# Performance work log

Hardware: AMD Instinct MI355X
Metric: run time of the kernel (lower is better)

The kernel has to match this reference:

```python
import jax, jax.numpy as jnp
import numpy as np

NUM_HEADS = 8
EMBED = 512
HEAD_DIM = EMBED // NUM_HEADS
B, S = 4, 2048


def setup_inputs() -> dict:
    key = jax.random.key(0)
    ks = jax.random.split(key, 8)
    sc = 0.02
    return {
        "values": jax.random.normal(ks[0], (B, S, EMBED), dtype=jnp.float32),
        "keys": jax.random.normal(ks[1], (B, S, EMBED), dtype=jnp.float32),
        "query": jax.random.normal(ks[2], (B, S, EMBED), dtype=jnp.float32),
        "Wv": jax.random.normal(ks[3], (HEAD_DIM, HEAD_DIM), dtype=jnp.float32) * sc,
        "Wk": jax.random.normal(ks[4], (HEAD_DIM, HEAD_DIM), dtype=jnp.float32) * sc,
        "Wq": jax.random.normal(ks[5], (HEAD_DIM, HEAD_DIM), dtype=jnp.float32) * sc,
        "Wo": jax.random.normal(ks[6], (EMBED, EMBED), dtype=jnp.float32) * sc,
        "bo": jnp.zeros((EMBED,), dtype=jnp.float32),
    }


def reference(values, keys, query, Wv, Wk, Wq, Wo, bo):
    b, s, _ = query.shape
    # split heads: [B, S, H, D]
    v = values.reshape(b, s, NUM_HEADS, HEAD_DIM)
    k = keys.reshape(b, s, NUM_HEADS, HEAD_DIM)
    q = query.reshape(b, s, NUM_HEADS, HEAD_DIM)
    # per-head linear (nn.Linear: x @ W.T), weights shared across heads
    v = jnp.einsum("bshd,ed->bshe", v, Wv)
    k = jnp.einsum("bshd,ed->bshe", k, Wk)
    q = jnp.einsum("bshd,ed->bshe", q, Wq)
    # energy: [B, H, Q, K]
    energy = jnp.einsum("bqhd,bkhd->bhqk", q, k)
    # NOTE: original scales by sqrt(embed_size), not sqrt(head_dim)
    attn = jax.nn.softmax(energy / jnp.sqrt(jnp.float32(EMBED)), axis=-1)
    out = jnp.einsum("bhqk,bkhd->bqhd", attn, v).reshape(b, s, EMBED)
    return out @ Wo.T + bo
```

## Files before the change

### kernel.cpp

```cpp
#include <hip/hip_runtime.h>

#define H 8
#define D 64
#define E 512
#define BATCH 4
#define SEQ 2048

typedef __bf16 bf16v8 __attribute__((ext_vector_type(8)));
typedef float f32v4 __attribute__((ext_vector_type(4)));
typedef unsigned int u32v4 __attribute__((ext_vector_type(4)));
typedef unsigned short u16v4 __attribute__((ext_vector_type(4)));

#define MFMA16(a,b,c) __builtin_amdgcn_mfma_f32_16x16x32_bf16(a,b,c,0,0,0)

#define AS1 __attribute__((address_space(1)))
#define AS3 __attribute__((address_space(3)))
#define GLDS16(g, l) __builtin_amdgcn_global_load_lds((const AS1 void*)(g), (AS3 void*)(l), 16, 0, 0)

static __device__ __forceinline__ unsigned short f2bf(float f) {
  unsigned u = __builtin_bit_cast(unsigned, f);
  u += 0x7fffu + ((u >> 16) & 1u);
  return (unsigned short)(u >> 16);
}

static __device__ __forceinline__ float exp2_hw(float x) {
#if __has_builtin(__builtin_amdgcn_exp2f)
  return __builtin_amdgcn_exp2f(x);
#else
  return exp2f(x);
#endif
}

static __device__ __forceinline__ bf16v8 lds16(const char* p) {
  return __builtin_bit_cast(bf16v8, *(const u32v4*)p);
}

__global__ void prep_w(const float* __restrict__ Wo, const float* __restrict__ Wv,
                       const float* __restrict__ Wq, const float* __restrict__ Wk,
                       unsigned short* __restrict__ Wo2, unsigned short* __restrict__ MT) {
  int bx = blockIdx.x;
  if (bx < 1024) {
    int i = bx * 256 + threadIdx.x;
    int n = i >> 9, c = i & 511;
    int h = c >> 6, d = c & 63;
    float acc = 0.f;
    for (int e = 0; e < 64; ++e) acc += Wo[n*512 + h*64 + e] * Wv[e*64 + d];
    Wo2[n*512 + c] = f2bf(acc);
  } else {
    int i = (bx - 1024) * 256 + threadIdx.x;
    int d2 = i >> 6, d1 = i & 63;
    float acc = 0.f;
    for (int e = 0; e < 64; ++e) acc += Wq[e*64 + d1] * Wk[e*64 + d2];
    MT[d2*64 + d1] = f2bf(acc * 0.04419417382415922f);
  }
}

__global__ void prep_tok(const float* __restrict__ v, const float* __restrict__ keys,
                         unsigned short* __restrict__ vT, unsigned short* __restrict__ kb) {
  __shared__ float tile[64][65];
  int bh = blockIdx.y;
  int b = bh >> 3, h = bh & 7;
  int sc = blockIdx.x;
  int t = threadIdx.x;
  int flat = bh * 32 + sc;
  {
    const float* kp = keys + (size_t)flat * 4096;
    unsigned short* ko = kb + (size_t)flat * 4096;
    #pragma unroll
    for (int i = 0; i < 4; ++i) {
      f32v4 x = *(const f32v4*)(kp + (i*256 + t)*4);
      u16v4 o = { f2bf(x[0]), f2bf(x[1]), f2bf(x[2]), f2bf(x[3]) };
      *(u16v4*)(ko + (i*256 + t)*4) = o;
    }
  }
  #pragma unroll
  for (int i = 0; i < 16; ++i) {
    int idx = i*256 + t; int si = idx >> 6, d = idx & 63;
    tile[si][d] = v[((size_t)(b*SEQ + sc*64 + si))*E + h*64 + d];
  }
  __syncthreads();
  #pragma unroll
  for (int i = 0; i < 16; ++i) {
    int idx = i*256 + t; int d = idx >> 6, si = idx & 63;
    vT[((size_t)(bh*64 + d))*SEQ + sc*64 + si] = f2bf(tile[si][d]);
  }
}

__global__ __launch_bounds__(256, 4) void attn(const float* __restrict__ query,
                                               const unsigned short* __restrict__ MT,
                                               const unsigned short* __restrict__ kb,
                                               const unsigned short* __restrict__ vT,
                                               unsigned short* __restrict__ ao) {
  __shared__ __align__(16) char lds[40960];
  int bh = blockIdx.y, b = bh >> 3, h = bh & 7;
  int qt = blockIdx.x;
  int tid = threadIdx.x, w = tid >> 6, lane = tid & 63, hi = lane >> 4, lo = lane & 15;
  char* pw = lds + 32768 + w*2048;

  const unsigned short* kbase = kb + (size_t)(b*SEQ)*E + h*64;
  const unsigned short* vbase = vT + (size_t)bh*64*SEQ;

  int srow = tid >> 3, scc = tid & 7;

  #pragma unroll
  for (int i = 0; i < 2; ++i) {
    int row = i*32 + srow;
    int sc = scc ^ (row & 7);
    GLDS16(kbase + (size_t)row*E + sc*8,   lds        + i*4096 + w*1024);
    GLDS16(vbase + (size_t)row*SEQ + sc*8, lds + 8192 + i*4096 + w*1024);
  }
  {
    char* xl = lds + 16384;
    char* ml = lds + 24576;
    #pragma unroll
    for (int i = 0; i < 4; ++i) {
      int c = i*256 + tid;
      int row = c >> 4, cc = c & 15;
      f32v4 xv = *(const f32v4*)(query + (size_t)(b*SEQ + qt*64 + row)*E + h*64 + cc*4);
      u16v4 o = { f2bf(xv[0]), f2bf(xv[1]), f2bf(xv[2]), f2bf(xv[3]) };
      int off = row*128 + ((((cc >> 1) ^ (row & 7))) << 4) + (cc & 1)*8;
      *(u16v4*)(xl + off) = o;
    }
    #pragma unroll
    for (int i = 0; i < 2; ++i) {
      int c = i*256 + tid; int row = c >> 3, cc = c & 7;
      *(u32v4*)(ml + row*128 + ((cc ^ (row & 7)) << 4)) = *(const u32v4*)(MT + row*64 + cc*8);
    }
  }
  __syncthreads();

  bf16v8 qa[2];
  {
    char* xl = lds + 16384;
    char* ml = lds + 24576;
    f32v4 acc[4] = {};
    #pragma unroll
    for (int kk = 0; kk < 2; ++kk) {
      int arow = w*16 + lo;
      bf16v8 af = lds16(xl + arow*128 + (((kk*4 + hi) ^ (arow & 7)) << 4));
      #pragma unroll
      for (int nt = 0; nt < 4; ++nt) {
        int brow = nt*16 + lo;
        bf16v8 bf_ = lds16(ml + brow*128 + (((kk*4 + hi) ^ (brow & 7)) << 4));
        acc[nt] = MFMA16(af, bf_, acc[nt]);
      }
    }
    #pragma unroll
    for (int nt = 0; nt < 4; ++nt)
      #pragma unroll
      for (int r = 0; r < 4; ++r) {
        int qrw = 4*hi + r;
        *(unsigned short*)(pw + qrw*128 + ((nt*32 + lo*2) ^ ((qrw & 7) << 4))) = f2bf(acc[nt][r]);
      }
    asm volatile("s_waitcnt lgkmcnt(0)" ::: "memory");
    __builtin_amdgcn_sched_barrier(0);
    qa[0] = lds16(pw + lo*128 + (((0*4 + hi) ^ (lo & 7)) << 4));
    qa[1] = lds16(pw + lo*128 + (((1*4 + hi) ^ (lo & 7)) << 4));
  }
  __syncthreads();

  f32v4 oacc[4] = {};
  float lsum[4] = {0.f, 0.f, 0.f, 0.f};

  for (int kt = 0; kt < 32; ++kt) {
    const char* klc = lds + (kt & 1)*16384;
    const char* vlc = klc + 8192;
    if (kt < 31) {
      char* kln = lds + ((kt & 1) ^ 1)*16384;
      char* vln = kln + 8192;
      #pragma unroll
      for (int i = 0; i < 2; ++i) {
        int row = i*32 + srow;
        int sc = scc ^ (row & 7);
        GLDS16(kbase + (size_t)((kt+1)*64 + row)*E + sc*8, kln + i*4096 + w*1024);
        GLDS16(vbase + (size_t)row*SEQ + (kt+1)*64 + sc*8, vln + i*4096 + w*1024);
      }
    }
    f32v4 sacc[4] = {};
    #pragma unroll
    for (int nt = 0; nt < 4; ++nt)
      #pragma unroll
      for (int kk = 0; kk < 2; ++kk) {
        int row = nt*16 + lo;
        bf16v8 kf = lds16(klc + row*128 + (((kk*4 + hi) ^ (row & 7)) << 4));
        sacc[nt] = MFMA16(qa[kk], kf, sacc[nt]);
      }
    #pragma unroll
    for (int nt = 0; nt < 4; ++nt)
      #pragma unroll
      for (int r = 0; r < 4; ++r) {
        float p = exp2_hw(sacc[nt][r] * 1.4426950408889634f);
        lsum[r] += p;
        int qrw = 4*hi + r;
        *(unsigned short*)(pw + qrw*128 + ((nt*32 + lo*2) ^ ((qrw & 7) << 4))) = f2bf(p);
      }
    asm volatile("s_waitcnt lgkmcnt(0)" ::: "memory");
    __builtin_amdgcn_sched_barrier(0);
    #pragma unroll
    for (int ks = 0; ks < 2; ++ks) {
      bf16v8 pa = lds16(pw + lo*128 + (((ks*4 + hi) ^ (lo & 7)) << 4));
      #pragma unroll
      for (int dt = 0; dt < 4; ++dt) {
        int row = dt*16 + lo;
        bf16v8 vf = lds16(vlc + row*128 + (((ks*4 + hi) ^ (row & 7)) << 4));
        oacc[dt] = MFMA16(pa, vf, oacc[dt]);
      }
    }
    __syncthreads();
  }
  #pragma unroll
  for (int r = 0; r < 4; ++r) {
    #pragma unroll
    for (int m = 1; m < 16; m <<= 1) lsum[r] += __shfl_xor(lsum[r], m, 64);
    lsum[r] = __builtin_amdgcn_rcpf(lsum[r]);
  }
  #pragma unroll
  for (int dt = 0; dt < 4; ++dt)
    #pragma unroll
    for (int r = 0; r < 4; ++r) {
      int tok = b*SEQ + qt*64 + w*16 + 4*hi + r;
      ao[(size_t)tok*E + h*64 + dt*16 + lo] = f2bf(oacc[dt][r] * lsum[r]);
    }
}

__global__ __launch_bounds__(256, 4) void final_gemm(const unsigned short* __restrict__ ao,
                                                     const unsigned short* __restrict__ wo2,
                                                     const float* __restrict__ bo,
                                                     float* __restrict__ out) {
  __shared__ __align__(16) char lds[32768];
  int m0 = blockIdx.x * 64, n0 = blockIdx.y * 64;
  int tid = threadIdx.x, w = tid >> 6, lane = tid & 63, hi = lane >> 4, lo = lane & 15;
  int wm = (w >> 1) * 32, wn = (w & 1) * 32;
  int srow = tid >> 3, scc = tid & 7;
  f32v4 acc[2][2] = {};
  #pragma unroll
  for (int i = 0; i < 2; ++i) {
    int row = i*32 + srow;
    int sc = scc ^ (row & 7);
    GLDS16(ao  + (size_t)(m0 + row)*E + sc*8, lds        + i*4096 + w*1024);
    GLDS16(wo2 + (size_t)(n0 + row)*E + sc*8, lds + 8192 + i*4096 + w*1024);
  }
  __syncthreads();
  for (int kt = 0; kt < 8; ++kt) {
    const char* al = lds + (kt & 1)*16384;
    const char* bl = al + 8192;
    if (kt < 7) {
      char* an = lds + ((kt & 1) ^ 1)*16384;
      char* bn = an + 8192;
      #pragma unroll
      for (int i = 0; i < 2; ++i) {
        int row = i*32 + srow;
        int sc = scc ^ (row & 7);
        GLDS16(ao  + (size_t)(m0 + row)*E + (kt+1)*64 + sc*8, an + i*4096 + w*1024);
        GLDS16(wo2 + (size_t)(n0 + row)*E + (kt+1)*64 + sc*8, bn + i*4096 + w*1024);
      }
    }
    #pragma unroll
    for (int kk = 0; kk < 2; ++kk) {
      bf16v8 af[2], bfv[2];
      #pragma unroll
      for (int mt = 0; mt < 2; ++mt) {
        int row = wm + mt*16 + lo;
        af[mt] = lds16(al + row*128 + (((kk*4 + hi) ^ (row & 7)) << 4));
      }
      #pragma unroll
      for (int nt = 0; nt < 2; ++nt) {
        int row = wn + nt*16 + lo;
        bfv[nt] = lds16(bl + row*128 + (((kk*4 + hi) ^ (row & 7)) << 4));
      }
      #pragma unroll
      for (int mt = 0; mt < 2; ++mt)
        #pragma unroll
        for (int nt = 0; nt < 2; ++nt)
          acc[mt][nt] = MFMA16(af[mt], bfv[nt], acc[mt][nt]);
    }
    __syncthreads();
  }
  #pragma unroll
  for (int nt = 0; nt < 2; ++nt) {
    float bias = bo[n0 + wn + nt*16 + lo];
    #pragma unroll
    for (int mt = 0; mt < 2; ++mt)
      #pragma unroll
      for (int r = 0; r < 4; ++r)
        out[(size_t)(m0 + wm + mt*16 + 4*hi + r)*E + n0 + wn + nt*16 + lo] =
            acc[mt][nt][r] + bias;
  }
}

extern "C" void kernel_launch(void* const* d_in, const int* in_sizes, int n_in,
                              void* d_out, int out_size, void* d_ws, size_t ws_size,
                              hipStream_t stream) {
  const float* values = (const float*)d_in[0];
  const float* keys   = (const float*)d_in[1];
  const float* query  = (const float*)d_in[2];
  const float* Wv     = (const float*)d_in[3];
  const float* Wk     = (const float*)d_in[4];
  const float* Wq     = (const float*)d_in[5];
  const float* Wo     = (const float*)d_in[6];
  const float* bo     = (const float*)d_in[7];
  float* out = (float*)d_out;
  char* ws = (char*)d_ws;

  unsigned short* MT  = (unsigned short*)(ws);
  unsigned short* Wo2 = (unsigned short*)(ws + 8192);
  unsigned short* kb  = (unsigned short*)(ws + (1u  << 20));
  unsigned short* vT  = (unsigned short*)(ws + (9u  << 20));
  unsigned short* ao  = (unsigned short*)(ws + (17u << 20));

  prep_w    <<<1040, 256, 0, stream>>>(Wo, Wv, Wq, Wk, Wo2, MT);
  prep_tok  <<<dim3(32, 32), 256, 0, stream>>>(values, keys, vT, kb);
  attn      <<<dim3(32, 32), 256, 0, stream>>>(query, MT, kb, vT, ao);
  final_gemm<<<dim3(128, 8), 256, 0, stream>>>(ao, Wo2, bo, out);
}
```

Measured before the change: 178.2 us.

## Merge prep kernels, double query tile per attention block, enlarge GEMM tiles

Merges the two preprocessing kernels into a single launch. The attention kernel now handles 128 queries per block (32 rows per wave), so each K/V tile loaded into LDS is reused twice as much, at the cost of more registers and LDS and half as many blocks. The output GEMM moves to 128x128 tiles, and s_setprio is raised around the MFMA sections. Fewer blocks (512 for attention, 256 for the GEMM) may leave some of the MI355X's compute units underused.

Result: faster. 171.4 us (-3.8%).

```diff
diff --git a/kernel.cpp b/kernel.cpp
--- a/kernel.cpp
+++ b/kernel.cpp
@@ -35,71 +35,68 @@
   return __builtin_bit_cast(bf16v8, *(const u32v4*)p);
 }
 
-__global__ void prep_w(const float* __restrict__ Wo, const float* __restrict__ Wv,
-                       const float* __restrict__ Wq, const float* __restrict__ Wk,
-                       unsigned short* __restrict__ Wo2, unsigned short* __restrict__ MT) {
+__global__ void prep_all(const float* __restrict__ Wo, const float* __restrict__ Wv,
+                         const float* __restrict__ Wq, const float* __restrict__ Wk,
+                         const float* __restrict__ v, const float* __restrict__ keys,
+                         unsigned short* __restrict__ Wo2, unsigned short* __restrict__ MT,
+                         unsigned short* __restrict__ vT, unsigned short* __restrict__ kb) {
+  __shared__ float tile[64][65];
   int bx = blockIdx.x;
+  int t = threadIdx.x;
   if (bx < 1024) {
-    int i = bx * 256 + threadIdx.x;
+    int i = bx * 256 + t;
     int n = i >> 9, c = i & 511;
     int h = c >> 6, d = c & 63;
     float acc = 0.f;
     for (int e = 0; e < 64; ++e) acc += Wo[n*512 + h*64 + e] * Wv[e*64 + d];
     Wo2[n*512 + c] = f2bf(acc);
-  } else {
-    int i = (bx - 1024) * 256 + threadIdx.x;
+  } else if (bx < 1040) {
+    int i = (bx - 1024) * 256 + t;
     int d2 = i >> 6, d1 = i & 63;
     float acc = 0.f;
     for (int e = 0; e < 64; ++e) acc += Wq[e*64 + d1] * Wk[e*64 + d2];
     MT[d2*64 + d1] = f2bf(acc * 0.04419417382415922f);
-  }
-}
-
-__global__ void prep_tok(const float* __restrict__ v, const float* __restrict__ keys,
-                         unsigned short* __restrict__ vT, unsigned short* __restrict__ kb) {
-  __shared__ float tile[64][65];
-  int bh = blockIdx.y;
-  int b = bh >> 3, h = bh & 7;
-  int sc = blockIdx.x;
-  int t = threadIdx.x;
-  int flat = bh * 32 + sc;
-  {
-    const float* kp = keys + (size_t)flat * 4096;
-    unsigned short* ko = kb + (size_t)flat * 4096;
-    #pragma unroll
-    for (int i = 0; i < 4; ++i) {
-      f32v4 x = *(const f32v4*)(kp + (i*256 + t)*4);
-      u16v4 o = { f2bf(x[0]), f2bf(x[1]), f2bf(x[2]), f2bf(x[3]) };
-      *(u16v4*)(ko + (i*256 + t)*4) = o;
-    }
-  }
-  #pragma unroll
-  for (int i = 0; i < 16; ++i) {
-    int idx = i*256 + t; int si = idx >> 6, d = idx & 63;
-    tile[si][d] = v[((size_t)(b*SEQ + sc*64 + si))*E + h*64 + d];
-  }
-  __syncthreads();
-  #pragma unroll
-  for (int i = 0; i < 16; ++i) {
-    int idx = i*256 + t; int d = idx >> 6, si = idx & 63;
-    vT[((size_t)(bh*64 + d))*SEQ + sc*64 + si] = f2bf(tile[si][d]);
-  }
-}
-
-__global__ __launch_bounds__(256, 4) void attn(const float* __restrict__ query,
+  } else {
+    int flat = bx - 1040;
+    int bh = flat >> 5, sc = flat & 31;
+    int b = bh >> 3, h = bh & 7;
+    {
+      const float* kp = keys + (size_t)flat * 4096;
+      unsigned short* ko = kb + (size_t)flat * 4096;
+      #pragma unroll
+      for (int i = 0; i < 4; ++i) {
+        f32v4 x = *(const f32v4*)(kp + (i*256 + t)*4);
+        u16v4 o = { f2bf(x[0]), f2bf(x[1]), f2bf(x[2]), f2bf(x[3]) };
+        *(u16v4*)(ko + (i*256 + t)*4) = o;
+      }
+    }
+    #pragma unroll
+    for (int i = 0; i < 16; ++i) {
+      int idx = i*256 + t; int si = idx >> 6, d = idx & 63;
+      tile[si][d] = v[((size_t)(b*SEQ + sc*64 + si))*E + h*64 + d];
+    }
+    __syncthreads();
+    #pragma unroll
+    for (int i = 0; i < 16; ++i) {
+      int idx = i*256 + t; int d = idx >> 6, si = idx & 63;
+      vT[((size_t)(bh*64 + d))*SEQ + sc*64 + si] = f2bf(tile[si][d]);
+    }
+  }
+}
+
+__global__ __launch_bounds__(256, 2) void attn(const float* __restrict__ query,
                                                const unsigned short* __restrict__ MT,
                                                const unsigned short* __restrict__ kb,
                                                const unsigned short* __restrict__ vT,
                                                unsigned short* __restrict__ ao) {
-  __shared__ __align__(16) char lds[40960];
+  __shared__ __align__(16) char lds[49152];
   int bh = blockIdx.y, b = bh >> 3, h = bh & 7;
   int qt = blockIdx.x;
   int tid = threadIdx.x, w = tid >> 6, lane = tid & 63, hi = lane >> 4, lo = lane & 15;
-  char* pw = lds + 32768 + w*2048;
+  char* pw = lds + 32768 + w*4096;
 
   const unsigned short* kbase = kb + (size_t)(b*SEQ)*E + h*64;
   const unsigned short* vbase = vT + (size_t)bh*64*SEQ;
-
   int srow = tid >> 3, scc = tid & 7;
 
   #pragma unroll
@@ -111,12 +108,12 @@
   }
   {
     char* xl = lds + 16384;
-    char* ml = lds + 24576;
-    #pragma unroll
-    for (int i = 0; i < 4; ++i) {
+    char* ml = lds + 32768;
+    #pragma unroll
+    for (int i = 0; i < 8; ++i) {
       int c = i*256 + tid;
       int row = c >> 4, cc = c & 15;
-      f32v4 xv = *(const f32v4*)(query + (size_t)(b*SEQ + qt*64 + row)*E + h*64 + cc*4);
+      f32v4 xv = *(const f32v4*)(query + (size_t)(b*SEQ + qt*128 + row)*E + h*64 + cc*4);
       u16v4 o = { f2bf(xv[0]), f2bf(xv[1]), f2bf(xv[2]), f2bf(xv[3]) };
       int off = row*128 + ((((cc >> 1) ^ (row & 7))) << 4) + (cc & 1)*8;
       *(u16v4*)(xl + off) = o;
@@ -129,158 +126,181 @@
   }
   __syncthreads();
 
-  bf16v8 qa[2];
+  bf16v8 qa[2][2];
   {
     char* xl = lds + 16384;
-    char* ml = lds + 24576;
-    f32v4 acc[4] = {};
-    #pragma unroll
-    for (int kk = 0; kk < 2; ++kk) {
-      int arow = w*16 + lo;
-      bf16v8 af = lds16(xl + arow*128 + (((kk*4 + hi) ^ (arow & 7)) << 4));
-      #pragma unroll
-      for (int nt = 0; nt < 4; ++nt) {
-        int brow = nt*16 + lo;
-        bf16v8 bf_ = lds16(ml + brow*128 + (((kk*4 + hi) ^ (brow & 7)) << 4));
-        acc[nt] = MFMA16(af, bf_, acc[nt]);
-      }
-    }
-    #pragma unroll
-    for (int nt = 0; nt < 4; ++nt)
-      #pragma unroll
-      for (int r = 0; r < 4; ++r) {
-        int qrw = 4*hi + r;
-        *(unsigned short*)(pw + qrw*128 + ((nt*32 + lo*2) ^ ((qrw & 7) << 4))) = f2bf(acc[nt][r]);
-      }
+    char* ml = lds + 32768;
+    f32v4 qacc[2][4] = {};
+    #pragma unroll
+    for (int kk = 0; kk < 2; ++kk)
+      #pragma unroll
+      for (int mrep = 0; mrep < 2; ++mrep) {
+        int arow = w*32 + mrep*16 + lo;
+        bf16v8 af = lds16(xl + arow*128 + (((kk*4 + hi) ^ (arow & 7)) << 4));
+        #pragma unroll
+        for (int nt = 0; nt < 4; ++nt) {
+          int brow = nt*16 + lo;
+          bf16v8 bf_ = lds16(ml + brow*128 + (((kk*4 + hi) ^ (brow & 7)) << 4));
+          qacc[mrep][nt] = MFMA16(af, bf_, qacc[mrep][nt]);
+        }
+      }
+    __syncthreads();
+    #pragma unroll
+    for (int mrep = 0; mrep < 2; ++mrep)
+      #pragma unroll
+      for (int nt = 0; nt < 4; ++nt)
+        #pragma unroll
+        for (int r = 0; r < 4; ++r) {
+          int qrw = mrep*16 + 4*hi + r;
+          *(unsigned short*)(pw + qrw*128 + ((nt*32 + lo*2) ^ ((qrw & 7) << 4))) =
+              f2bf(qacc[mrep][nt][r]);
+        }
     asm volatile("s_waitcnt lgkmcnt(0)" ::: "memory");
     __builtin_amdgcn_sched_barrier(0);
-    qa[0] = lds16(pw + lo*128 + (((0*4 + hi) ^ (lo & 7)) << 4));
-    qa[1] = lds16(pw + lo*128 + (((1*4 + hi) ^ (lo & 7)) << 4));
-  }
-  __syncthreads();
-
-  f32v4 oacc[4] = {};
-  float lsum[4] = {0.f, 0.f, 0.f, 0.f};
+    #pragma unroll
+    for (int mrep = 0; mrep < 2; ++mrep)
+      #pragma unroll
+      for (int kk = 0; kk < 2; ++kk) {
+        int row = mrep*16 + lo;
+        qa[mrep][kk] = lds16(pw + row*128 + (((kk*4 + hi) ^ (lo & 7)) << 4));
+      }
+  }
+
+  f32v4 oacc[2][4] = {};
+  float lsum[2][4] = {};
 
   for (int kt = 0; kt < 32; ++kt) {
     const char* klc = lds + (kt & 1)*16384;
     const char* vlc = klc + 8192;
     if (kt < 31) {
       char* kln = lds + ((kt & 1) ^ 1)*16384;
-      char* vln = kln + 8192;
       #pragma unroll
       for (int i = 0; i < 2; ++i) {
         int row = i*32 + srow;
         int sc = scc ^ (row & 7);
-        GLDS16(kbase + (size_t)((kt+1)*64 + row)*E + sc*8, kln + i*4096 + w*1024);
-        GLDS16(vbase + (size_t)row*SEQ + (kt+1)*64 + sc*8, vln + i*4096 + w*1024);
-      }
-    }
-    f32v4 sacc[4] = {};
+        GLDS16(kbase + (size_t)((kt+1)*64 + row)*E + sc*8, kln        + i*4096 + w*1024);
+        GLDS16(vbase + (size_t)row*SEQ + (kt+1)*64 + sc*8, kln + 8192 + i*4096 + w*1024);
+      }
+    }
+    f32v4 sacc[2][4] = {};
+    __builtin_amdgcn_s_setprio(1);
     #pragma unroll
     for (int nt = 0; nt < 4; ++nt)
       #pragma unroll
       for (int kk = 0; kk < 2; ++kk) {
         int row = nt*16 + lo;
         bf16v8 kf = lds16(klc + row*128 + (((kk*4 + hi) ^ (row & 7)) << 4));
-        sacc[nt] = MFMA16(qa[kk], kf, sacc[nt]);
-      }
-    #pragma unroll
-    for (int nt = 0; nt < 4; ++nt)
-      #pragma unroll
-      for (int r = 0; r < 4; ++r) {
-        float p = exp2_hw(sacc[nt][r] * 1.4426950408889634f);
-        lsum[r] += p;
-        int qrw = 4*hi + r;
-        *(unsigned short*)(pw + qrw*128 + ((nt*32 + lo*2) ^ ((qrw & 7) << 4))) = f2bf(p);
-      }
+        sacc[0][nt] = MFMA16(qa[0][kk], kf, sacc[0][nt]);
+        sacc[1][nt] = MFMA16(qa[1][kk], kf, sacc[1][nt]);
+      }
+    __builtin_amdgcn_s_setprio(0);
+    #pragma unroll
+    for (int mrep = 0; mrep < 2; ++mrep)
+      #pragma unroll
+      for (int nt = 0; nt < 4; ++nt)
+        #pragma unroll
+        for (int r = 0; r < 4; ++r) {
+          float p = exp2_hw(sacc[mrep][nt][r] * 1.4426950408889634f);
+          lsum[mrep][r] += p;
+          int qrw = mrep*16 + 4*hi + r;
+          *(unsigned short*)(pw + qrw*128 + ((nt*32 + lo*2) ^ ((qrw & 7) << 4))) = f2bf(p);
+        }
     asm volatile("s_waitcnt lgkmcnt(0)" ::: "memory");
     __builtin_amdgcn_sched_barrier(0);
+    __builtin_amdgcn_s_setprio(1);
     #pragma unroll
     for (int ks = 0; ks < 2; ++ks) {
-      bf16v8 pa = lds16(pw + lo*128 + (((ks*4 + hi) ^ (lo & 7)) << 4));
+      bf16v8 pa0 = lds16(pw + lo*128        + (((ks*4 + hi) ^ (lo & 7)) << 4));
+      bf16v8 pa1 = lds16(pw + (16+lo)*128   + (((ks*4 + hi) ^ (lo & 7)) << 4));
       #pragma unroll
       for (int dt = 0; dt < 4; ++dt) {
         int row = dt*16 + lo;
         bf16v8 vf = lds16(vlc + row*128 + (((ks*4 + hi) ^ (row & 7)) << 4));
-        oacc[dt] = MFMA16(pa, vf, oacc[dt]);
-      }
-    }
+        oacc[0][dt] = MFMA16(pa0, vf, oacc[0][dt]);
+        oacc[1][dt] = MFMA16(pa1, vf, oacc[1][dt]);
+      }
+    }
+    __builtin_amdgcn_s_setprio(0);
     __syncthreads();
   }
   #pragma unroll
-  for (int r = 0; r < 4; ++r) {
-    #pragma unroll
-    for (int m = 1; m < 16; m <<= 1) lsum[r] += __shfl_xor(lsum[r], m, 64);
-    lsum[r] = __builtin_amdgcn_rcpf(lsum[r]);
-  }
-  #pragma unroll
-  for (int dt = 0; dt < 4; ++dt)
+  for (int mrep = 0; mrep < 2; ++mrep)
     #pragma unroll
     for (int r = 0; r < 4; ++r) {
-      int tok = b*SEQ + qt*64 + w*16 + 4*hi + r;
-      ao[(size_t)tok*E + h*64 + dt*16 + lo] = f2bf(oacc[dt][r] * lsum[r]);
-    }
-}
-
-__global__ __launch_bounds__(256, 4) void final_gemm(const unsigned short* __restrict__ ao,
+      #pragma unroll
+      for (int m = 1; m < 16; m <<= 1) lsum[mrep][r] += __shfl_xor(lsum[mrep][r], m, 64);
+      lsum[mrep][r] = __builtin_amdgcn_rcpf(lsum[mrep][r]);
+    }
+  #pragma unroll
+  for (int mrep = 0; mrep < 2; ++mrep)
+    #pragma unroll
+    for (int dt = 0; dt < 4; ++dt)
+      #pragma unroll
+      for (int r = 0; r < 4; ++r) {
+        int tok = b*SEQ + qt*128 + w*32 + mrep*16 + 4*hi + r;
+        ao[(size_t)tok*E + h*64 + dt*16 + lo] = f2bf(oacc[mrep][dt][r] * lsum[mrep][r]);
+      }
+}
+
+__global__ __launch_bounds__(256, 2) void final_gemm(const unsigned short* __restrict__ ao,
                                                      const unsigned short* __restrict__ wo2,
                                                      const float* __restrict__ bo,
                                                      float* __restrict__ out) {
-  __shared__ __align__(16) char lds[32768];
-  int m0 = blockIdx.x * 64, n0 = blockIdx.y * 64;
+  __shared__ __align__(16) char lds[65536];
+  int m0 = blockIdx.x * 128, n0 = blockIdx.y * 128;
   int tid = threadIdx.x, w = tid >> 6, lane = tid & 63, hi = lane >> 4, lo = lane & 15;
-  int wm = (w >> 1) * 32, wn = (w & 1) * 32;
+  int wm = (w >> 1) * 64, wn = (w & 1) * 64;
   int srow = tid >> 3, scc = tid & 7;
-  f32v4 acc[2][2] = {};
-  #pragma unroll
-  for (int i = 0; i < 2; ++i) {
+  f32v4 acc[4][4] = {};
+  #pragma unroll
+  for (int i = 0; i < 4; ++i) {
     int row = i*32 + srow;
     int sc = scc ^ (row & 7);
-    GLDS16(ao  + (size_t)(m0 + row)*E + sc*8, lds        + i*4096 + w*1024);
-    GLDS16(wo2 + (size_t)(n0 + row)*E + sc*8, lds + 8192 + i*4096 + w*1024);
+    GLDS16(ao  + (size_t)(m0 + row)*E + sc*8, lds         + i*4096 + w*1024);
+    GLDS16(wo2 + (size_t)(n0 + row)*E + sc*8, lds + 16384 + i*4096 + w*1024);
   }
   __syncthreads();
   for (int kt = 0; kt < 8; ++kt) {
-    const char* al = lds + (kt & 1)*16384;
-    const char* bl = al + 8192;
+    const char* al = lds + (kt & 1)*32768;
+    const char* bl = al + 16384;
     if (kt < 7) {
-      char* an = lds + ((kt & 1) ^ 1)*16384;
-      char* bn = an + 8192;
-      #pragma unroll
-      for (int i = 0; i < 2; ++i) {
+      char* an = lds + ((kt & 1) ^ 1)*32768;
+      #pragma unroll
+      for (int i = 0; i < 4; ++i) {
         int row = i*32 + srow;
         int sc = scc ^ (row & 7);
-        GLDS16(ao  + (size_t)(m0 + row)*E + (kt+1)*64 + sc*8, an + i*4096 + w*1024);
-        GLDS16(wo2 + (size_t)(n0 + row)*E + (kt+1)*64 + sc*8, bn + i*4096 + w*1024);
-      }
-    }
+        GLDS16(ao  + (size_t)(m0 + row)*E + (kt+1)*64 + sc*8, an         + i*4096 + w*1024);
+        GLDS16(wo2 + (size_t)(n0 + row)*E + (kt+1)*64 + sc*8, an + 16384 + i*4096 + w*1024);
+      }
+    }
+    __builtin_amdgcn_s_setprio(1);
     #pragma unroll
     for (int kk = 0; kk < 2; ++kk) {
-      bf16v8 af[2], bfv[2];
-      #pragma unroll
-      for (int mt = 0; mt < 2; ++mt) {
+      bf16v8 af[4], bfv[4];
+      #pragma unroll
+      for (int mt = 0; mt < 4; ++mt) {
         int row = wm + mt*16 + lo;
         af[mt] = lds16(al + row*128 + (((kk*4 + hi) ^ (row & 7)) << 4));
       }
       #pragma unroll
-      for (int nt = 0; nt < 2; ++nt) {
+      for (int nt = 0; nt < 4; ++nt) {
         int row = wn + nt*16 + lo;
         bfv[nt] = lds16(bl + row*128 + (((kk*4 + hi) ^ (row & 7)) << 4));
       }
       #pragma unroll
-      for (int mt = 0; mt < 2; ++mt)
+      for (int mt = 0; mt < 4; ++mt)
         #pragma unroll
-        for (int nt = 0; nt < 2; ++nt)
+        for (int nt = 0; nt < 4; ++nt)
           acc[mt][nt] = MFMA16(af[mt], bfv[nt], acc[mt][nt]);
     }
+    __builtin_amdgcn_s_setprio(0);
     __syncthreads();
   }
   #pragma unroll
-  for (int nt = 0; nt < 2; ++nt) {
+  for (int nt = 0; nt < 4; ++nt) {
     float bias = bo[n0 + wn + nt*16 + lo];
     #pragma unroll
-    for (int mt = 0; mt < 2; ++mt)
+    for (int mt = 0; mt < 4; ++mt)
       #pragma unroll
       for (int r = 0; r < 4; ++r)
         out[(size_t)(m0 + wm + mt*16 + 4*hi + r)*E + n0 + wn + nt*16 + lo] =
@@ -308,8 +328,7 @@
   unsigned short* vT  = (unsigned short*)(ws + (9u  << 20));
   unsigned short* ao  = (unsigned short*)(ws + (17u << 20));
 
-  prep_w    <<<1040, 256, 0, stream>>>(Wo, Wv, Wq, Wk, Wo2, MT);
-  prep_tok  <<<dim3(32, 32), 256, 0, stream>>>(values, keys, vT, kb);
-  attn      <<<dim3(32, 32), 256, 0, stream>>>(query, MT, kb, vT, ao);
-  final_gemm<<<dim3(128, 8), 256, 0, stream>>>(ao, Wo2, bo, out);
-}
+  prep_all  <<<2064, 256, 0, stream>>>(Wo, Wv, Wq, Wk, values, keys, Wo2, MT, vT, kb);
+  attn      <<<dim3(16, 32), 256, 0, stream>>>(query, MT, kb, vT, ao);
+  final_gemm<<<dim3(64, 4),  256, 0, stream>>>(ao, Wo2, bo, out);
+}
```
